# Performance work log

Measured on AMD Instinct MI355X. Metric: run time of the kernel, lower is better.

Reference implementation:

```python
import jax, jax.numpy as jnp
import numpy as np

LN_EPS = 1e-5


def setup_inputs() -> dict:
    key = jax.random.key(0)
    k1, k2 = jax.random.split(key)
    n, c, t, v = 64, 256, 128, 25
    inner2 = 512  # 2 * hidden_dim * n_heads
    return {
        "x": jax.random.normal(k1, (n, c, t, v), dtype=jnp.float32),
        "ln_gamma": jnp.ones((c,), dtype=jnp.float32),
        "ln_beta": jnp.zeros((c,), dtype=jnp.float32),
        "W": jax.random.normal(k2, (inner2, c), dtype=jnp.float32),
        "b": jnp.zeros((inner2,), dtype=jnp.float32),
        "n_heads": 8,
    }


def reference(x, ln_gamma, ln_beta, W, b, n_heads):
    n, c, t, v = x.shape
    inner2 = W.shape[0]
    d = inner2 // 2 // n_heads  # per-head dim
    scale = d ** (-0.5)

    # n c t v -> n t v c
    y = jnp.transpose(x, (0, 2, 3, 1))
    # LayerNorm over channel dim
    mu = jnp.mean(y, axis=-1, keepdims=True)
    var = jnp.mean(jnp.square(y - mu), axis=-1, keepdims=True)
    y = (y - mu) * jax.lax.rsqrt(var + LN_EPS) * ln_gamma + ln_beta
    # QK projection: (n, t, v, 2*h*d)
    y = jnp.einsum('ntvc,ec->ntve', y, W) + b
    q, k = jnp.split(y, 2, axis=-1)

    def heads(z):
        # (n, t, v, h*d) -> (n*t, h, v, d)
        z = z.reshape(n * t, v, n_heads, d)
        return jnp.transpose(z, (0, 2, 1, 3))

    q, k = heads(q), heads(k)
    dots = jnp.einsum('bhid,bhjd->bhij', q, k) * scale
    attn = jax.nn.softmax(dots, axis=-1).astype(jnp.float32)
    return attn
```

## Files before the change

kernel.cpp:

```cpp
#include <hip/hip_runtime.h>
#include <math.h>
#include <stdint.h>

typedef _Float16 f16x8 __attribute__((ext_vector_type(8)));
typedef float    f32x4 __attribute__((ext_vector_type(4)));

#define NB    8192
#define V_    25
#define KS_   0.25505003938643f

__global__ __launch_bounds__(256)
void prep_w(const float* __restrict__ W, _Float16* __restrict__ ws) {
    int tid  = blockIdx.x * 256 + threadIdx.x;
    int lane = tid & 63;
    int idx  = tid >> 6;
    int C    = idx >> 4;
    int T2   = idx & 15;
    int half = C >> 3, ch = C & 7;
    int l15  = lane & 15, q4 = lane >> 4;
    const float* src = W + (size_t)(half*256 + T2*16 + l15) * 256 + ch*32 + q4*8;
    f16x8 hi, lo;
    #pragma unroll
    for (int j = 0; j < 8; ++j) {
        float w = src[j];
        _Float16 hh = (_Float16)w;
        hi[j] = hh;
        lo[j] = (_Float16)(w - (float)hh);
    }
    char* base = (char*)ws + (size_t)idx * 2048 + lane * 16;
    *(f16x8*)base          = hi;
    *(f16x8*)(base + 1024) = lo;
}

struct __align__(16) SMem {
    union {
        struct {
            _Float16 ysh[32][264];
            _Float16 ysl[32][264];
        } g;
        _Float16 qk[4][2][32][64];
    } u;
    float s_mu[32];
    float s_rs[32];
};

__global__ __launch_bounds__(256, 4)
void fused_ln_qk_attn(const float* __restrict__ x,
                      const float* __restrict__ gamma,
                      const float* __restrict__ beta,
                      const _Float16* __restrict__ wsp,
                      const float* __restrict__ bias,
                      float* __restrict__ out)
{
    __shared__ SMem sm;

    const int tid  = threadIdx.x;
    const int lane = tid & 63;
    const int wv   = tid >> 6;
    const int l15  = lane & 15;
    const int q4   = lane >> 4;
    const int nt   = blockIdx.x;
    const int n    = nt >> 7;
    const int t    = nt & 127;
    const int base = n * 819200 + t * 25;

    float xv[V_];
    {
        const float* xr = x + base + tid * 3200;
        #pragma unroll
        for (int v = 0; v < V_; ++v) xv[v] = xr[v];
        #pragma unroll
        for (int v = 0; v < V_; ++v) {
            _Float16 h = (_Float16)xv[v];
            sm.u.g.ysh[v][tid] = h;
            sm.u.g.ysl[v][tid] = (_Float16)(xv[v] - (float)h);
        }
    }
    __syncthreads();

    {
        const int v = tid >> 3;
        const int j = tid & 7;
        float s1 = 0.0f, s2 = 0.0f;
        #pragma unroll
        for (int m2 = 0; m2 < 4; ++m2) {
            f16x8 hv = *(const f16x8*)&sm.u.g.ysh[v][j*32 + m2*8];
            f16x8 lv = *(const f16x8*)&sm.u.g.ysl[v][j*32 + m2*8];
            #pragma unroll
            for (int e = 0; e < 8; ++e) {
                float val = (float)hv[e] + (float)lv[e];
                s1 += val; s2 += val * val;
            }
        }
        s1 += __shfl_xor(s1, 1); s2 += __shfl_xor(s2, 1);
        s1 += __shfl_xor(s1, 2); s2 += __shfl_xor(s2, 2);
        s1 += __shfl_xor(s1, 4); s2 += __shfl_xor(s2, 4);
        if (j == 0) {
            if (v < V_) {
                float mu  = s1 * (1.0f/256.0f);
                float var = s2 * (1.0f/256.0f) - mu * mu;
                sm.s_mu[v] = mu;
                sm.s_rs[v] = rsqrtf(var + 1e-5f);
            } else { sm.s_mu[v] = 0.0f; sm.s_rs[v] = 0.0f; }
        }
    }
    __syncthreads();

    {
        const float g  = gamma[tid];
        const float be = beta[tid];
        #pragma unroll
        for (int v = 0; v < V_; ++v) {
            float val = (xv[v] - sm.s_mu[v]) * sm.s_rs[v] * g + be;
            _Float16 h = (_Float16)val;
            sm.u.g.ysh[v][tid] = h;
            sm.u.g.ysl[v][tid] = (_Float16)(val - (float)h);
        }
    }
    __syncthreads();

    float bv[2][4];
    #pragma unroll
    for (int h = 0; h < 2; ++h)
        #pragma unroll
        for (int j = 0; j < 4; ++j)
            bv[h][j] = bias[h*256 + (wv*4 + j)*16 + l15];

    f32x4 acc[2][2][4];
    #pragma unroll
    for (int h = 0; h < 2; ++h)
        #pragma unroll
        for (int m = 0; m < 2; ++m)
            #pragma unroll
            for (int j = 0; j < 4; ++j)
                acc[h][m][j] = (f32x4){0.f, 0.f, 0.f, 0.f};

    const char* bbase = (const char*)wsp + (size_t)lane * 16 + (size_t)(wv*4) * 2048;

    for (int ch = 0; ch < 8; ++ch) {
        const int kb = ch*32 + q4*8;
        f16x8 Ah0 = *(const f16x8*)&sm.u.g.ysh[l15][kb];
        f16x8 Ah1 = *(const f16x8*)&sm.u.g.ysh[16 + l15][kb];
        f16x8 Al0 = *(const f16x8*)&sm.u.g.ysl[l15][kb];
        f16x8 Al1 = *(const f16x8*)&sm.u.g.ysl[16 + l15][kb];
        #pragma unroll
        for (int half = 0; half < 2; ++half) {
            const char* cb = bbase + (size_t)(half*8 + ch) * 16 * 2048;
            #pragma unroll
            for (int j = 0; j < 4; ++j) {
                const char* pj = cb + (size_t)j * 2048;
                f16x8 Bh = *(const f16x8*)pj;
                f16x8 Bl = *(const f16x8*)(pj + 1024);
                acc[half][0][j] = __builtin_amdgcn_mfma_f32_16x16x32_f16(Ah0, Bh, acc[half][0][j], 0, 0, 0);
                acc[half][0][j] = __builtin_amdgcn_mfma_f32_16x16x32_f16(Al0, Bh, acc[half][0][j], 0, 0, 0);
                acc[half][0][j] = __builtin_amdgcn_mfma_f32_16x16x32_f16(Ah0, Bl, acc[half][0][j], 0, 0, 0);
                acc[half][1][j] = __builtin_amdgcn_mfma_f32_16x16x32_f16(Ah1, Bh, acc[half][1][j], 0, 0, 0);
                acc[half][1][j] = __builtin_amdgcn_mfma_f32_16x16x32_f16(Al1, Bh, acc[half][1][j], 0, 0, 0);
                acc[half][1][j] = __builtin_amdgcn_mfma_f32_16x16x32_f16(Ah1, Bl, acc[half][1][j], 0, 0, 0);
            }
        }
    }
    __syncthreads();

    char* qh = (char*)&sm.u.qk[wv][0][0][0];
    char* ql = (char*)&sm.u.qk[wv][1][0][0];

    #pragma unroll
    for (int hh = 0; hh < 2; ++hh) {
        #pragma unroll
        for (int half = 0; half < 2; ++half)
            #pragma unroll
            for (int jj = 0; jj < 2; ++jj) {
                const int  j   = 2*hh + jj;
                const float bb = bv[half][j];
                const int  col = half*32 + jj*16 + l15;
                #pragma unroll
                for (int mt = 0; mt < 2; ++mt)
                    #pragma unroll
                    for (int r = 0; r < 4; ++r) {
                        const int row = mt*16 + q4*4 + r;
                        const int off = (row*128 + col*2) ^ ((row & 7) << 4);
                        float val  = acc[half][mt][j][r] + bb;
                        _Float16 h = (_Float16)val;
                        *(_Float16*)(qh + off) = h;
                        *(_Float16*)(ql + off) = (_Float16)(val - (float)h);
                    }
            }

        f16x8 Kh[2], Kl[2], Qh[2], Ql[2];
        #pragma unroll
        for (int tt = 0; tt < 2; ++tt) {
            const int rr  = tt*16 + l15;
            const int swz = (rr & 7) << 4;
            const int oK  = (rr*128 + 64 + q4*16) ^ swz;
            const int oQ  = (rr*128 +      q4*16) ^ swz;
            Kh[tt] = *(const f16x8*)(qh + oK);
            Kl[tt] = *(const f16x8*)(ql + oK);
            Qh[tt] = *(const f16x8*)(qh + oQ);
            Ql[tt] = *(const f16x8*)(ql + oQ);
        }

        f32x4 D[2][2];
        #pragma unroll
        for (int jt = 0; jt < 2; ++jt)
            #pragma unroll
            for (int it = 0; it < 2; ++it) {
                f32x4 d = (f32x4){0.f, 0.f, 0.f, 0.f};
                d = __builtin_amdgcn_mfma_f32_16x16x32_f16(Kh[jt], Qh[it], d, 0, 0, 0);
                d = __builtin_amdgcn_mfma_f32_16x16x32_f16(Kl[jt], Qh[it], d, 0, 0, 0);
                d = __builtin_amdgcn_mfma_f32_16x16x32_f16(Kh[jt], Ql[it], d, 0, 0, 0);
                D[jt][it] = d;
            }

        float* op = out + (size_t)nt * 5000 + (wv*2 + hh) * 625;
        #pragma unroll
        for (int it = 0; it < 2; ++it) {
            const int i = it*16 + l15;
            float pv[2][4];
            float mx = -3.0e38f;
            #pragma unroll
            for (int jt = 0; jt < 2; ++jt)
                #pragma unroll
                for (int r = 0; r < 4; ++r) {
                    const int j = jt*16 + q4*4 + r;
                    float v = (j < V_) ? D[jt][it][r] : -3.0e38f;
                    pv[jt][r] = v;
                    mx = fmaxf(mx, v);
                }
            mx = fmaxf(mx, __shfl_xor(mx, 16));
            mx = fmaxf(mx, __shfl_xor(mx, 32));
            float sum = 0.0f;
            #pragma unroll
            for (int jt = 0; jt < 2; ++jt)
                #pragma unroll
                for (int r = 0; r < 4; ++r) {
                    float e = exp2f((pv[jt][r] - mx) * KS_);
                    pv[jt][r] = e;
                    sum += e;
                }
            sum += __shfl_xor(sum, 16);
            sum += __shfl_xor(sum, 32);
            const float rcp = 1.0f / sum;
            if (i < V_) {
                #pragma unroll
                for (int jt = 0; jt < 2; ++jt)
                    #pragma unroll
                    for (int r = 0; r < 4; ++r) {
                        const int j = jt*16 + q4*4 + r;
                        if (j < V_) op[i*25 + j] = pv[jt][r] * rcp;
                    }
            }
        }
    }
}

extern "C" void kernel_launch(void* const* d_in, const int* in_sizes, int n_in,
                              void* d_out, int out_size, void* d_ws, size_t ws_size,
                              hipStream_t stream) {
    const float* x     = (const float*)d_in[0];
    const float* gamma = (const float*)d_in[1];
    const float* beta  = (const float*)d_in[2];
    const float* W     = (const float*)d_in[3];
    const float* b     = (const float*)d_in[4];
    _Float16* wsp = (_Float16*)d_ws;
    float* out = (float*)d_out;

    prep_w<<<dim3(64), dim3(256), 0, stream>>>(W, wsp);
    fused_ln_qk_attn<<<dim3(NB), dim3(256), 0, stream>>>(x, gamma, beta, wsp, b, out);
}
```

Measured before the change: 542.1 us.

## Fold LayerNorm affine and normalization into GEMM epilogue, shrink shared memory

```diff
diff --git a/kernel.cpp b/kernel.cpp
--- a/kernel.cpp
+++ b/kernel.cpp
@@ -10,46 +10,64 @@
 #define KS_   0.25505003938643f
 
 __global__ __launch_bounds__(256)
-void prep_w(const float* __restrict__ W, _Float16* __restrict__ ws) {
-    int tid  = blockIdx.x * 256 + threadIdx.x;
-    int lane = tid & 63;
-    int idx  = tid >> 6;
-    int C    = idx >> 4;
-    int T2   = idx & 15;
-    int half = C >> 3, ch = C & 7;
-    int l15  = lane & 15, q4 = lane >> 4;
-    const float* src = W + (size_t)(half*256 + T2*16 + l15) * 256 + ch*32 + q4*8;
-    f16x8 hi, lo;
-    #pragma unroll
-    for (int j = 0; j < 8; ++j) {
-        float w = src[j];
-        _Float16 hh = (_Float16)w;
-        hi[j] = hh;
-        lo[j] = (_Float16)(w - (float)hh);
-    }
-    char* base = (char*)ws + (size_t)idx * 2048 + lane * 16;
-    *(f16x8*)base          = hi;
-    *(f16x8*)(base + 1024) = lo;
+void prep_w(const float* __restrict__ W, const float* __restrict__ gamma,
+            const float* __restrict__ beta, const float* __restrict__ bias,
+            char* __restrict__ ws) {
+    const int blk = blockIdx.x;
+    if (blk < 64) {
+        int tid  = blk * 256 + threadIdx.x;
+        int lane = tid & 63;
+        int idx  = tid >> 6;
+        int C    = idx >> 4;
+        int T2   = idx & 15;
+        int half = C >> 3, ch = C & 7;
+        int l15  = lane & 15, q4 = lane >> 4;
+        int col0 = ch*32 + q4*8;
+        const float* src = W + (size_t)(half*256 + T2*16 + l15) * 256 + col0;
+        f16x8 hi, lo;
+        #pragma unroll
+        for (int j = 0; j < 8; ++j) {
+            float w = src[j] * gamma[col0 + j];
+            _Float16 hh = (_Float16)w;
+            hi[j] = hh;
+            lo[j] = (_Float16)(w - (float)hh);
+        }
+        char* base = ws + (size_t)idx * 2048 + lane * 16;
+        *(f16x8*)base          = hi;
+        *(f16x8*)(base + 1024) = lo;
+    } else {
+        int e = (blk - 64) * 256 + threadIdx.x;
+        const float* wr = W + (size_t)e * 256;
+        float a1 = 0.f, a2 = 0.f;
+        #pragma unroll 8
+        for (int c = 0; c < 256; ++c) {
+            float w = wr[c];
+            a1 += w * gamma[c];
+            a2 += w * beta[c];
+        }
+        a2 += bias[e];
+        ((float*)(ws + 512*1024))[e]        = a1;
+        ((float*)(ws + 512*1024 + 2048))[e] = a2;
+    }
 }
 
 struct __align__(16) SMem {
     union {
         struct {
-            _Float16 ysh[32][264];
-            _Float16 ysl[32][264];
+            _Float16 ysh[25][256];
+            _Float16 ysl[25][256];
         } g;
-        _Float16 qk[4][2][32][64];
+        _Float16 qk[4][2][25][64];
     } u;
     float s_mu[32];
     float s_rs[32];
 };
 
-__global__ __launch_bounds__(256, 4)
+__global__ __launch_bounds__(256, 5)
 void fused_ln_qk_attn(const float* __restrict__ x,
-                      const float* __restrict__ gamma,
-                      const float* __restrict__ beta,
                       const _Float16* __restrict__ wsp,
-                      const float* __restrict__ bias,
+                      const float* __restrict__ s1p,
+                      const float* __restrict__ s2p,
                       float* __restrict__ out)
 {
     __shared__ SMem sm;
@@ -64,67 +82,60 @@
     const int t    = nt & 127;
     const int base = n * 819200 + t * 25;
 
-    float xv[V_];
+    char* yh = (char*)&sm.u.g.ysh[0][0];
+    char* yl = yh + 12800;
+
     {
         const float* xr = x + base + tid * 3200;
         #pragma unroll
-        for (int v = 0; v < V_; ++v) xv[v] = xr[v];
-        #pragma unroll
         for (int v = 0; v < V_; ++v) {
-            _Float16 h = (_Float16)xv[v];
-            sm.u.g.ysh[v][tid] = h;
-            sm.u.g.ysl[v][tid] = (_Float16)(xv[v] - (float)h);
+            float val = xr[v];
+            _Float16 h = (_Float16)val;
+            const int off = (v*512 + tid*2) ^ ((v & 7) << 4);
+            *(_Float16*)(yh + off) = h;
+            *(_Float16*)(yl + off) = (_Float16)(val - (float)h);
         }
     }
     __syncthreads();
 
     {
-        const int v = tid >> 3;
-        const int j = tid & 7;
-        float s1 = 0.0f, s2 = 0.0f;
+        const int v  = tid >> 3;
+        const int vc = v < 24 ? v : 24;
+        const int j  = tid & 7;
+        float a1 = 0.f, a2 = 0.f;
         #pragma unroll
         for (int m2 = 0; m2 < 4; ++m2) {
-            f16x8 hv = *(const f16x8*)&sm.u.g.ysh[v][j*32 + m2*8];
-            f16x8 lv = *(const f16x8*)&sm.u.g.ysl[v][j*32 + m2*8];
+            const int off = (vc*512 + (j*32 + m2*8)*2) ^ ((vc & 7) << 4);
+            f16x8 hv = *(const f16x8*)(yh + off);
+            f16x8 lv = *(const f16x8*)(yl + off);
             #pragma unroll
             for (int e = 0; e < 8; ++e) {
                 float val = (float)hv[e] + (float)lv[e];
-                s1 += val; s2 += val * val;
-            }
-        }
-        s1 += __shfl_xor(s1, 1); s2 += __shfl_xor(s2, 1);
-        s1 += __shfl_xor(s1, 2); s2 += __shfl_xor(s2, 2);
-        s1 += __shfl_xor(s1, 4); s2 += __shfl_xor(s2, 4);
+                a1 += val; a2 += val * val;
+            }
+        }
+        a1 += __shfl_xor(a1, 1); a2 += __shfl_xor(a2, 1);
+        a1 += __shfl_xor(a1, 2); a2 += __shfl_xor(a2, 2);
+        a1 += __shfl_xor(a1, 4); a2 += __shfl_xor(a2, 4);
         if (j == 0) {
             if (v < V_) {
-                float mu  = s1 * (1.0f/256.0f);
-                float var = s2 * (1.0f/256.0f) - mu * mu;
+                float mu  = a1 * (1.0f/256.0f);
+                float var = a2 * (1.0f/256.0f) - mu * mu;
                 sm.s_mu[v] = mu;
                 sm.s_rs[v] = rsqrtf(var + 1e-5f);
             } else { sm.s_mu[v] = 0.0f; sm.s_rs[v] = 0.0f; }
         }
     }
-    __syncthreads();
-
-    {
-        const float g  = gamma[tid];
-        const float be = beta[tid];
-        #pragma unroll
-        for (int v = 0; v < V_; ++v) {
-            float val = (xv[v] - sm.s_mu[v]) * sm.s_rs[v] * g + be;
-            _Float16 h = (_Float16)val;
-            sm.u.g.ysh[v][tid] = h;
-            sm.u.g.ysl[v][tid] = (_Float16)(val - (float)h);
-        }
-    }
-    __syncthreads();
-
-    float bv[2][4];
+
+    float sv1[2][4], sv2[2][4];
     #pragma unroll
     for (int h = 0; h < 2; ++h)
         #pragma unroll
-        for (int j = 0; j < 4; ++j)
-            bv[h][j] = bias[h*256 + (wv*4 + j)*16 + l15];
+        for (int j = 0; j < 4; ++j) {
+            const int e = h*256 + (wv*4 + j)*16 + l15;
+            sv1[h][j] = s1p[e];
+            sv2[h][j] = s2p[e];
+        }
 
     f32x4 acc[2][2][4];
     #pragma unroll
@@ -136,13 +147,15 @@
                 acc[h][m][j] = (f32x4){0.f, 0.f, 0.f, 0.f};
 
     const char* bbase = (const char*)wsp + (size_t)lane * 16 + (size_t)(wv*4) * 2048;
-
+    const int r1 = (16 + l15) < 24 ? (16 + l15) : 24;
     for (int ch = 0; ch < 8; ++ch) {
-        const int kb = ch*32 + q4*8;
-        f16x8 Ah0 = *(const f16x8*)&sm.u.g.ysh[l15][kb];
-        f16x8 Ah1 = *(const f16x8*)&sm.u.g.ysh[16 + l15][kb];
-        f16x8 Al0 = *(const f16x8*)&sm.u.g.ysl[l15][kb];
-        f16x8 Al1 = *(const f16x8*)&sm.u.g.ysl[16 + l15][kb];
+        const int kb = (ch*32 + q4*8) * 2;
+        const int o0 = (l15*512 + kb) ^ ((l15 & 7) << 4);
+        const int o1 = (r1 *512 + kb) ^ ((r1  & 7) << 4);
+        f16x8 Ah0 = *(const f16x8*)(yh + o0);
+        f16x8 Ah1 = *(const f16x8*)(yh + o1);
+        f16x8 Al0 = *(const f16x8*)(yl + o0);
+        f16x8 Al1 = *(const f16x8*)(yl + o1);
         #pragma unroll
         for (int half = 0; half < 2; ++half) {
             const char* cb = bbase + (size_t)(half*8 + ch) * 16 * 2048;
@@ -162,8 +175,14 @@
     }
     __syncthreads();
 
+    f32x4 mu4[2], rs4[2];
+    mu4[0] = *(const f32x4*)&sm.s_mu[q4*4];
+    mu4[1] = *(const f32x4*)&sm.s_mu[16 + q4*4];
+    rs4[0] = *(const f32x4*)&sm.s_rs[q4*4];
+    rs4[1] = *(const f32x4*)&sm.s_rs[16 + q4*4];
+
     char* qh = (char*)&sm.u.qk[wv][0][0][0];
-    char* ql = (char*)&sm.u.qk[wv][1][0][0];
+    char* ql = qh + 3200;
 
     #pragma unroll
     for (int hh = 0; hh < 2; ++hh) {
@@ -171,26 +190,30 @@
         for (int half = 0; half < 2; ++half)
             #pragma unroll
             for (int jj = 0; jj < 2; ++jj) {
-                const int  j   = 2*hh + jj;
-                const float bb = bv[half][j];
+                const int   j  = 2*hh + jj;
+                const float c1 = sv1[half][j];
+                const float c2 = sv2[half][j];
                 const int  col = half*32 + jj*16 + l15;
                 #pragma unroll
                 for (int mt = 0; mt < 2; ++mt)
                     #pragma unroll
                     for (int r = 0; r < 4; ++r) {
                         const int row = mt*16 + q4*4 + r;
-                        const int off = (row*128 + col*2) ^ ((row & 7) << 4);
-                        float val  = acc[half][mt][j][r] + bb;
-                        _Float16 h = (_Float16)val;
-                        *(_Float16*)(qh + off) = h;
-                        *(_Float16*)(ql + off) = (_Float16)(val - (float)h);
+                        if (row < V_) {
+                            float tv  = fmaf(-mu4[mt][r], c1, acc[half][mt][j][r]);
+                            float val = fmaf(rs4[mt][r], tv, c2);
+                            _Float16 h = (_Float16)val;
+                            const int off = (row*128 + col*2) ^ ((row & 7) << 4);
+                            *(_Float16*)(qh + off) = h;
+                            *(_Float16*)(ql + off) = (_Float16)(val - (float)h);
+                        }
                     }
             }
 
         f16x8 Kh[2], Kl[2], Qh[2], Ql[2];
         #pragma unroll
         for (int tt = 0; tt < 2; ++tt) {
-            const int rr  = tt*16 + l15;
+            int rr = tt*16 + l15; if (rr > 24) rr = 24;
             const int swz = (rr & 7) << 4;
             const int oK  = (rr*128 + 64 + q4*16) ^ swz;
             const int oQ  = (rr*128 +      q4*16) ^ swz;
@@ -262,9 +285,13 @@
     const float* beta  = (const float*)d_in[2];
     const float* W     = (const float*)d_in[3];
     const float* b     = (const float*)d_in[4];
-    _Float16* wsp = (_Float16*)d_ws;
+    char* ws = (char*)d_ws;
     float* out = (float*)d_out;
 
-    prep_w<<<dim3(64), dim3(256), 0, stream>>>(W, wsp);
-    fused_ln_qk_attn<<<dim3(NB), dim3(256), 0, stream>>>(x, gamma, beta, wsp, b, out);
+    prep_w<<<dim3(66), dim3(256), 0, stream>>>(W, gamma, beta, b, ws);
+    fused_ln_qk_attn<<<dim3(NB), dim3(256), 0, stream>>>(
+        x, (const _Float16*)ws,
+        (const float*)(ws + 512*1024),
+        (const float*)(ws + 512*1024 + 2048),
+        out);
 }
```

After: 912.3 us. +68.3%, slower.
